# Performance work log

Hardware: AMD Instinct MI355X
Metric: run time of the kernel (lower is better)

Reference implementation:

```python
import itertools
import jax, jax.numpy as jnp
import numpy as np

B, N, ETA, K, Z, HID, NATOM, NBOND = 128, 40, 64, 32, 32, 256, 24, 5
A = B * N
E = B * (N * (N - 1) // 2)
TAU = 1.0  # gumbel_softmax_temperature default


def _bn(x, g, b, eps=1e-5):
    # BatchNorm1d in training mode: batch statistics, biased variance
    m = jnp.mean(x, axis=0)
    v = jnp.var(x, axis=0)
    return (x - m) * jax.lax.rsqrt(v + eps) * g + b


def _prelu(x, a):
    return jnp.where(x >= 0, x, a * x)


def _mlp(x, w1, b1, g, be, a, w2, b2):
    # Linear -> BatchNorm1d -> PReLU -> Linear
    return _prelu(_bn(x @ w1 + b1, g, be), a) @ w2 + b2


def setup_inputs() -> dict:
    key = jax.random.key(0)
    ks = jax.random.split(key, 16)
    # static all-pairs edge index per graph, offset per graph (mirrors decode_z)
    pairs = np.array(list(itertools.combinations(range(N), 2)), dtype=np.int64)  # [P,2]
    offs = (np.arange(B, dtype=np.int64) * N)[:, None, None]
    edge_index = jnp.asarray((pairs[None] + offs).reshape(-1, 2))  # [E,2]
    node_graph_idx = jnp.asarray(np.repeat(np.arange(B, dtype=np.int64), N))  # [A]

    def w(k, shape, fan_in):
        return jax.random.normal(k, shape, jnp.float32) / np.sqrt(fan_in).astype(np.float32)

    return {
        "eta": jax.random.normal(ks[0], (B, ETA), jnp.float32),
        "gumbel_u": jax.random.uniform(ks[1], (A, K), jnp.float32, 1e-6, 1.0 - 1e-6),
        "noise_z": jax.random.normal(ks[2], (A, Z), jnp.float32),
        "edge_index": edge_index,
        "node_graph_idx": node_graph_idx,
        # cluster_mlp
        "cw1": w(ks[3], (ETA, HID), ETA), "cb1": jnp.zeros(HID), "cg": jnp.ones(HID), "cbe": jnp.zeros(HID), "ca": jnp.float32(0.25),
        "cw2": w(ks[4], (HID, K), HID), "cb2": jnp.zeros(K),
        # mixture params (torch: randn means, zero log-sigmas)
        "cm": jax.random.normal(ks[5], (K, Z), jnp.float32), "cls": jnp.zeros((K, Z), jnp.float32),
        # atom_classifier
        "aw1": w(ks[6], (Z, HID), Z), "ab1": jnp.zeros(HID), "ag": jnp.ones(HID), "abe": jnp.zeros(HID), "aa": jnp.float32(0.25),
        "aw2": w(ks[7], (HID, NATOM), HID), "ab2": jnp.zeros(NATOM),
        # bond bilinear tensor [d, a, b]
        "bm": jax.random.normal(ks[8], (Z, Z, Z), jnp.float32) / np.sqrt(Z).astype(np.float32),
        # bond_type_mlp
        "bw1": w(ks[9], (Z, HID), Z), "bb1": jnp.zeros(HID), "bg": jnp.ones(HID), "bbe": jnp.zeros(HID), "ba": jnp.float32(0.25),
        "bw2": w(ks[10], (HID, NBOND), HID), "bb2": jnp.zeros(NBOND),
    }


def reference(eta, gumbel_u, noise_z, edge_index, node_graph_idx,
              cw1, cb1, cg, cbe, ca, cw2, cb2, cm, cls,
              aw1, ab1, ag, abe, aa, aw2, ab2,
              bm, bw1, bb1, bg, bbe, ba, bw2, bb2):
    # decode_eta: pi = softmax(cluster_mlp(eta)); log_pi = log(pi)
    log_pi = jax.nn.log_softmax(_mlp(eta, cw1, cb1, cg, cbe, ca, cw2, cb2), axis=1)
    # repeat_interleave(log_pi, num_atoms) -> per-atom logits
    logits = log_pi[node_graph_idx]  # [A, K]
    # gumbel_softmax hard=True (straight-through)
    g = -jnp.log(-jnp.log(gumbel_u))
    y_soft = jax.nn.softmax((logits + g) / TAU, axis=1)
    y_hard = jax.nn.one_hot(jnp.argmax(y_soft, axis=1), K, dtype=y_soft.dtype)
    c = y_hard - jax.lax.stop_gradient(y_soft) + y_soft  # [A, K]
    # select cluster mean / log-sigma, reparameterize
    mu = c @ cm                 # [A, Z]
    log_sigma = c @ cls         # [A, Z]
    z = noise_z * jnp.exp(jnp.clip(log_sigma, -20.0, 30.0)) + mu
    # decode_z
    atom_types = _mlp(z, aw1, ab1, ag, abe, aa, aw2, ab2)  # [A, NATOM]
    Wm = 0.5 * (bm + jnp.swapaxes(bm, 1, 2))  # symmetrize over (a, b)
    zi = z[edge_index[:, 0]]  # [E, Z]
    zj = z[edge_index[:, 1]]  # [E, Z]
    t = jnp.einsum('ea,dab->edb', zi, Wm)       # [E, Z, Z]
    edge_feat = jnp.einsum('edb,eb->ed', t, zj)  # z_i^T W_d z_j, [E, Z]
    edge_types = jax.nn.softmax(_mlp(edge_feat, bw1, bb1, bg, bbe, ba, bw2, bb2), axis=1)  # [E, NBOND]
    return atom_types, edge_types
```

## Files before the change

kernel.cpp:

```cpp
#include <hip/hip_runtime.h>
#include <math.h>

#define BG    128
#define NN    40
#define AK    32
#define ZD    32
#define HIDN  256
#define ETAD  64
#define NATOM 24
#define NBOND 5
#define NA    (BG*NN)
#define EPG   (NN*(NN-1)/2)
#define NE    (BG*EPG)

typedef __attribute__((ext_vector_type(8))) short bf16x8;
typedef __attribute__((ext_vector_type(4))) float f32x4;

__device__ __forceinline__ unsigned short f2bf(float f) {
    union { float f; unsigned int u; } x; x.f = f;
    unsigned int r = x.u + 0x7fffu + ((x.u >> 16) & 1u);
    return (unsigned short)(r >> 16);
}
__device__ __forceinline__ unsigned int pk2bf(float lo, float hi) {
    return (unsigned int)f2bf(lo) | ((unsigned int)f2bf(hi) << 16);
}

__global__ __launch_bounds__(256) void k_pre(const float* __restrict__ bm,
                                             const float* __restrict__ bw1,
                                             const float* __restrict__ aw1,
                                             const float* __restrict__ aw2,
                                             const float* __restrict__ eta,
                                             const float* __restrict__ cw1,
                                             const float* __restrict__ cb1,
                                             unsigned short* __restrict__ wmpk,
                                             unsigned short* __restrict__ bpack,
                                             unsigned short* __restrict__ apk1,
                                             unsigned short* __restrict__ apk2,
                                             float* __restrict__ h1,
                                             float* __restrict__ cpart,
                                             float* __restrict__ zacc) {
    int b = blockIdx.x, t = threadIdx.x;
    if (b < 128) {
        int idx = b*256 + t;
        int d = idx >> 10;
        int Bt = (idx >> 9) & 1, ln = (idx >> 3) & 63, j = idx & 7;
        int al = Bt*16 + (ln & 15);
        int be = (ln >> 4)*8 + j;
        float v = 0.5f * (bm[d*1024 + al*32 + be] + bm[d*1024 + be*32 + al]);
        wmpk[idx] = f2bf(v);
    } else if (b < 160) {
        int idx = (b - 128)*256 + t;
        int ct = idx >> 9, rem = idx & 511;
        int lane = rem >> 3, j = rem & 7;
        bpack[idx] = f2bf(bw1[((lane >> 4)*8 + j)*HIDN + ct*16 + (lane & 15)]);
    } else if (b < 192) {
        int idx = (b - 160)*256 + t;
        int ct = idx >> 9, rem = idx & 511;
        int lane = rem >> 3, j = rem & 7;
        apk1[idx] = f2bf(aw1[((lane >> 4)*8 + j)*HIDN + ct*16 + (lane & 15)]);
    } else if (b < 224) {
        int idx = (b - 192)*256 + t;
        int f = idx >> 9, rem = idx & 511;
        int lane = rem >> 3, j = rem & 7;
        int kc = f >> 1, ot = f & 1;
        int col = ot*16 + (lane & 15);
        int k = kc*32 + (lane >> 4)*8 + j;
        apk2[idx] = (col < NATOM) ? f2bf(aw2[k*NATOM + col]) : 0;
    } else if (b < 232) {
        __shared__ float es[16*ETAD];
        int b2 = b - 224;
        int r0 = b2*16;
        for (int i = t; i < 16*ETAD; i += 256) es[i] = eta[r0*ETAD + i];
        __syncthreads();
        int c = t;
        float bias = cb1[c], s = 0.f, ss = 0.f;
        for (int r = 0; r < 16; ++r) {
            float acc = bias;
#pragma unroll
            for (int a = 0; a < ETAD; ++a) acc += es[r*ETAD + a] * cw1[a*HIDN + c];
            h1[(r0 + r)*HIDN + c] = acc;
            s += acc; ss += acc*acc;
        }
        cpart[b2*512 + c] = s;
        cpart[b2*512 + 256 + c] = ss;
    } else {
        for (int i = t; i < 2112; i += 256) zacc[i] = 0.f;
    }
}

__global__ __launch_bounds__(256) void k_class_z(const float* __restrict__ h1,
                                                 const float* __restrict__ cpart,
                                                 const float* __restrict__ cg,
                                                 const float* __restrict__ cbe,
                                                 const float* __restrict__ ca,
                                                 const float* __restrict__ cw2,
                                                 const float* __restrict__ cb2,
                                                 const float* __restrict__ gum,
                                                 const float* __restrict__ noise,
                                                 const float* __restrict__ cm,
                                                 const float* __restrict__ cls,
                                                 float* __restrict__ z,
                                                 float* __restrict__ mom_z) {
    __shared__ float p[HIDN];
    __shared__ float vp2[256];
    __shared__ float oo[AK];
    __shared__ float lp[AK];
    __shared__ float zl[NN*36];
    int g = blockIdx.x, t = threadIdx.x;
    float aP = ca[0];
    {
        float s = 0.f, ss = 0.f;
#pragma unroll
        for (int b = 0; b < 8; ++b) { s += cpart[b*512 + t]; ss += cpart[b*512 + 256 + t]; }
        float m = s * (1.0f/(float)BG);
        float v = ss * (1.0f/(float)BG) - m*m;
        float x = h1[g*HIDN + t];
        float xn = (x - m) * (1.0f/sqrtf(v + 1e-5f)) * cg[t] + cbe[t];
        p[t] = xn >= 0.f ? xn : aP*xn;
    }
    __syncthreads();
    {
        int k = t & 31, part = t >> 5;
        float acc = 0.f;
        const float* pc = &p[part*32];
        const float* wc = &cw2[(part*32)*AK + k];
#pragma unroll
        for (int c = 0; c < 32; ++c) acc += pc[c] * wc[c*AK];
        vp2[t] = acc;
    }
    __syncthreads();
    if (t < AK) {
        float acc = cb2[t];
#pragma unroll
        for (int q = 0; q < 8; ++q) acc += vp2[q*32 + t];
        oo[t] = acc;
    }
    __syncthreads();
    if (t < AK) {
        float m = -INFINITY;
#pragma unroll
        for (int k = 0; k < AK; ++k) m = fmaxf(m, oo[k]);
        float S = 0.f;
#pragma unroll
        for (int k = 0; k < AK; ++k) S += expf(oo[k] - m);
        lp[t] = oo[t] - m - logf(S);
    }
    __syncthreads();
    int lane = t & 31;
#pragma unroll
    for (int nb = 0; nb < 5; ++nb) {
        int node = nb*8 + (t >> 5);
        int n = g*NN + node;
        float u = gum[(size_t)n*AK + lane];
        float x = lp[lane] - logf(-logf(u));
        float m = x;
#pragma unroll
        for (int s = 1; s < 32; s <<= 1) m = fmaxf(m, __shfl_xor(m, s, 32));
        float e = expf(x - m);
        float S = e;
#pragma unroll
        for (int s = 1; s < 32; s <<= 1) S += __shfl_xor(S, s, 32);
        unsigned long long bal = __ballot(x == m);
        unsigned grp = (unsigned)(bal >> (t & 32));
        int am = __ffs(grp) - 1;
        float best = 1.0f / S;
        float cam = (1.0f - best) + best;
        float ls = cam * cls[am*ZD + lane];
        ls = fminf(fmaxf(ls, -20.0f), 30.0f);
        float zv = noise[(size_t)n*ZD + lane]*expf(ls) + cam*cm[am*ZD + lane];
        z[(size_t)n*ZD + lane] = zv;
        zl[node*36 + lane] = zv;
    }
    __syncthreads();
    {
        int a = t >> 3, b4 = (t & 7) << 2;
        float ax = 0.f, ay = 0.f, az = 0.f, aw = 0.f;
        float mx = 0.f, my = 0.f, mz = 0.f, mw = 0.f;
        for (int r = 0; r < NN; ++r) {
            float  va = zl[r*36 + a];
            float4 vb = *(const float4*)&zl[r*36 + b4];
            ax += va*vb.x; ay += va*vb.y; az += va*vb.z; aw += va*vb.w;
            mx += vb.x;    my += vb.y;    mz += vb.z;    mw += vb.w;
        }
        atomicAdd(&mom_z[a*ZD + b4 + 0], ax);
        atomicAdd(&mom_z[a*ZD + b4 + 1], ay);
        atomicAdd(&mom_z[a*ZD + b4 + 2], az);
        atomicAdd(&mom_z[a*ZD + b4 + 3], aw);
        if (a == 0) {
            atomicAdd(&mom_z[ZD*ZD + b4 + 0], mx);
            atomicAdd(&mom_z[ZD*ZD + b4 + 1], my);
            atomicAdd(&mom_z[ZD*ZD + b4 + 2], mz);
            atomicAdd(&mom_z[ZD*ZD + b4 + 3], mw);
        }
    }
}

__global__ __launch_bounds__(256) void k_edge_feat(const float* __restrict__ z,
                                                   const unsigned short* __restrict__ wmpk,
                                                   float* __restrict__ ef) {
    __shared__ unsigned short zfrag[3*512];
    __shared__ unsigned short Tf[4][3*512];
    __shared__ float efl[EPG*9];
    int t = threadIdx.x;
    int g = blockIdx.x >> 2, dg = blockIdx.x & 3;

    if (t < 192) {
        int I = t >> 6, ln = t & 63;
        int row = I*16 + (ln & 15), c0 = (ln >> 4)*8;
        unsigned int pk[4] = {0u, 0u, 0u, 0u};
        if (row < NN) {
            const float* zp = &z[((size_t)g*NN + row)*ZD + c0];
            float4 v0 = *(const float4*)zp;
            float4 v1 = *(const float4*)(zp + 4);
            pk[0] = pk2bf(v0.x, v0.y); pk[1] = pk2bf(v0.z, v0.w);
            pk[2] = pk2bf(v1.x, v1.y); pk[3] = pk2bf(v1.z, v1.w);
        }
        *(uint4*)&zfrag[(I*64 + ln)*8] = make_uint4(pk[0], pk[1], pk[2], pk[3]);
    }
    __syncthreads();

    int w = t >> 6, lane = t & 63;
    int l15 = lane & 15, gq = lane >> 4;
    f32x4 zero4 = {0.f, 0.f, 0.f, 0.f};

    bf16x8 zf[3];
#pragma unroll
    for (int I = 0; I < 3; ++I) zf[I] = *(const bf16x8*)&zfrag[I*512 + lane*8];

    for (int dk = 0; dk < 2; ++dk) {
        int dd = w*2 + dk;
        int d  = dg*8 + dd;
        bf16x8 wA[2];
        wA[0] = *(const bf16x8*)&wmpk[(d*2 + 0)*512 + lane*8];
        wA[1] = *(const bf16x8*)&wmpk[(d*2 + 1)*512 + lane*8];

        unsigned short* tw = &Tf[w][0];
        int gqp_lo = (gq >> 1);
        int jo     = (gq & 1)*4;
#pragma unroll
        for (int Bt = 0; Bt < 2; ++Bt) {
#pragma unroll
            for (int I = 0; I < 3; ++I) {
                f32x4 c = __builtin_amdgcn_mfma_f32_16x16x32_bf16(wA[Bt], zf[I], zero4, 0, 0, 0);
                int gqp = Bt*2 + gqp_lo;
                int pos = I*512 + gqp*128 + l15*8 + jo;
                unsigned int d0 = pk2bf(c[0], c[1]);
                unsigned int d1 = pk2bf(c[2], c[3]);
                *(uint2*)&tw[pos] = make_uint2(d0, d1);
            }
        }
        __syncthreads();

        bf16x8 tf[3];
#pragma unroll
        for (int J = 0; J < 3; ++J) tf[J] = *(const bf16x8*)&Tf[w][J*512 + lane*8];

#pragma unroll
        for (int I = 0; I < 3; ++I) {
#pragma unroll
            for (int J = I; J < 3; ++J) {
                f32x4 gacc = __builtin_amdgcn_mfma_f32_16x16x32_bf16(zf[I], tf[J], zero4, 0, 0, 0);
                int j = J*16 + l15;
                if (j < NN) {
#pragma unroll
                    for (int r = 0; r < 4; ++r) {
                        int i = I*16 + 4*gq + r;
                        if (i < j) {
                            int e = i*(79 - i)/2 + (j - i - 1);
                            efl[e*9 + dd] = gacc[r];
                        }
                    }
                }
            }
        }
        __syncthreads();
    }

    size_t gE = (size_t)g * EPG;
    for (int idx = t; idx < EPG*8; idx += 256) {
        int e = idx >> 3, dd = idx & 7;
        ef[(gE + e)*ZD + dg*8 + dd] = efl[e*9 + dd];
    }
}

#define MOMB 192
__global__ __launch_bounds__(256) void k_moment(const float* __restrict__ src,
                                                float* __restrict__ mom, int nchunks) {
    __shared__ float sm[ZD*ZD + ZD];
    int t = threadIdx.x;
    for (int i = t; i < ZD*ZD + ZD; i += 256) sm[i] = 0.f;
    __syncthreads();
    int lane = t & 63, wv = t >> 6;
    int l15 = lane & 15, g4 = lane >> 4;
    int wgid = blockIdx.x * 4 + wv;
    const int nw = MOMB * 4;
    f32x4 aII = {0,0,0,0}, aIJ = {0,0,0,0}, aJI = {0,0,0,0}, aJJ = {0,0,0,0};
    float mI = 0.f, mJ = 0.f;
    for (int ch = wgid; ch < nchunks; ch += nw) {
        const float* p = src + ((size_t)ch*32 + g4*8)*ZD + l15;
        float vI[8], vJ[8];
#pragma unroll
        for (int j = 0; j < 8; ++j) { vI[j] = p[j*ZD]; vJ[j] = p[j*ZD + 16]; }
        bf16x8 fI, fJ;
#pragma unroll
        for (int j = 0; j < 8; ++j) {
            fI[j] = (short)f2bf(vI[j]); fJ[j] = (short)f2bf(vJ[j]);
            mI += vI[j]; mJ += vJ[j];
        }
        aII = __builtin_amdgcn_mfma_f32_16x16x32_bf16(fI, fI, aII, 0, 0, 0);
        aIJ = __builtin_amdgcn_mfma_f32_16x16x32_bf16(fI, fJ, aIJ, 0, 0, 0);
        aJI = __builtin_amdgcn_mfma_f32_16x16x32_bf16(fJ, fI, aJI, 0, 0, 0);
        aJJ = __builtin_amdgcn_mfma_f32_16x16x32_bf16(fJ, fJ, aJJ, 0, 0, 0);
    }
#pragma unroll
    for (int r = 0; r < 4; ++r) {
        int row = g4*4 + r;
        atomicAdd(&sm[row*ZD + l15],             aII[r]);
        atomicAdd(&sm[row*ZD + 16 + l15],        aIJ[r]);
        atomicAdd(&sm[(16 + row)*ZD + l15],      aJI[r]);
        atomicAdd(&sm[(16 + row)*ZD + 16 + l15], aJJ[r]);
    }
    atomicAdd(&sm[ZD*ZD + l15], mI);
    atomicAdd(&sm[ZD*ZD + 16 + l15], mJ);
    __syncthreads();
    for (int i = t; i < ZD*ZD + ZD; i += 256) atomicAdd(&mom[i], sm[i]);
}

__global__ __launch_bounds__(256) void k_prep2(const float* __restrict__ mom_z,
                                               const float* __restrict__ mom_ef,
                                               const float* __restrict__ aw1,
                                               const float* __restrict__ ab1,
                                               const float* __restrict__ ag,
                                               const float* __restrict__ abe,
                                               const float* __restrict__ bw1,
                                               const float* __restrict__ bb1,
                                               const float* __restrict__ bg,
                                               const float* __restrict__ bbe,
                                               float* __restrict__ ascale,
                                               float* __restrict__ ashift,
                                               float* __restrict__ bscale,
                                               float* __restrict__ bshift) {
    bool bond = blockIdx.x >= 8;
    const float* mom = bond ? mom_ef : mom_z;
    const float* w1  = bond ? bw1 : aw1;
    const float* b1  = bond ? bb1 : ab1;
    const float* g   = bond ? bg  : ag;
    const float* be  = bond ? bbe : abe;
    float inv_n      = bond ? (1.0f/(float)NE) : (1.0f/(float)NA);
    float* scale     = bond ? bscale : ascale;
    float* shift     = bond ? bshift : ashift;

    __shared__ float mean[ZD];
    __shared__ float cov[ZD*ZD];
    __shared__ float vp[256], mp[256];
    int t = threadIdx.x;
    if (t < ZD) mean[t] = mom[ZD*ZD + t] * inv_n;
    __syncthreads();
    for (int pp = t; pp < ZD*ZD; pp += 256) {
        int a = pp >> 5, b = pp & 31;
        cov[pp] = mom[pp] * inv_n - mean[a]*mean[b];
    }
    __syncthreads();
    int c = (blockIdx.x & 7) * 32 + (t & 31);
    int part = t >> 5;
    float wr[ZD];
#pragma unroll
    for (int b = 0; b < ZD; ++b) wr[b] = w1[b*HIDN + c];
    float var = 0.f, mh = 0.f;
#pragma unroll
    for (int q = 0; q < 4; ++q) {
        int a = part*4 + q;
        float tmp = 0.f;
#pragma unroll
        for (int b = 0; b < ZD; ++b) tmp += cov[a*ZD + b] * wr[b];
        var += tmp * wr[a];
        mh  += mean[a] * wr[a];
    }
    vp[t] = var; mp[t] = mh;
    __syncthreads();
    if (t < 32) {
        float v = 0.f, m = 0.f;
#pragma unroll
        for (int q = 0; q < 8; ++q) { v += vp[q*32 + t]; m += mp[q*32 + t]; }
        m += b1[c];
        float rs = rsqrtf(fmaxf(v, 0.f) + 1e-5f) * g[c];
        scale[c] = rs;
        shift[c] = be[c] - m * rs;
    }
}

#define PSH 264
#define ATOMB (NA/64)
#define BROWS4 128
__global__ __launch_bounds__(256) void k_out(const float* __restrict__ z,
                                             const unsigned short* __restrict__ apk1,
                                             const unsigned short* __restrict__ apk2,
                                             const float* __restrict__ ab1,
                                             const float* __restrict__ ascale,
                                             const float* __restrict__ ashift,
                                             const float* __restrict__ aa,
                                             const float* __restrict__ ab2,
                                             const float* __restrict__ ef,
                                             const unsigned short* __restrict__ bpack,
                                             const float* __restrict__ bb1,
                                             const float* __restrict__ bscale,
                                             const float* __restrict__ bshift,
                                             const float* __restrict__ ba,
                                             const float* __restrict__ bw2,
                                             const float* __restrict__ bb2,
                                             float* __restrict__ out_atom,
                                             float* __restrict__ out_bond) {
    __shared__ unsigned short smu[4*16*PSH];
    int t = threadIdx.x;
    int w = t >> 6, lane = t & 63;
    int l15 = lane & 15, gq = lane >> 4;
    f32x4 zero4 = {0.f, 0.f, 0.f, 0.f};

    if (blockIdx.x < ATOMB) {
        size_t r0 = (size_t)blockIdx.x * 64 + (size_t)w * 16;
        float aP = aa[0];
        unsigned short* ptw = &smu[w*16*PSH];

        const float* zp = &z[(r0 + l15)*ZD + gq*8];
        float4 z0 = *(const float4*)zp;
        float4 z1 = *(const float4*)(zp + 4);
        bf16x8 af;
        af[0] = (short)f2bf(z0.x); af[1] = (short)f2bf(z0.y);
        af[2] = (short)f2bf(z0.z); af[3] = (short)f2bf(z0.w);
        af[4] = (short)f2bf(z1.x); af[5] = (short)f2bf(z1.y);
        af[6] = (short)f2bf(z1.z); af[7] = (short)f2bf(z1.w);

#pragma unroll
        for (int ct = 0; ct < 16; ++ct) {
            bf16x8 bf = *(const bf16x8*)&apk1[ct*512 + lane*8];
            f32x4 c = __builtin_amdgcn_mfma_f32_16x16x32_bf16(af, bf, zero4, 0, 0, 0);
            int ch = ct*16 + l15;
            float sc = ascale[ch];
            float sh = ashift[ch] + ab1[ch]*sc;
#pragma unroll
            for (int r = 0; r < 4; ++r) {
                float xn = c[r]*sc + sh;
                float pv = xn >= 0.f ? xn : aP*xn;
                ptw[(4*gq + r)*PSH + ch] = f2bf(pv);
            }
        }

        f32x4 o0 = zero4, o1 = zero4;
#pragma unroll
        for (int kc = 0; kc < 8; ++kc) {
            bf16x8 af2 = *(const bf16x8*)&ptw[l15*PSH + kc*32 + gq*8];
            bf16x8 b0 = *(const bf16x8*)&apk2[(kc*2 + 0)*512 + lane*8];
            bf16x8 b1 = *(const bf16x8*)&apk2[(kc*2 + 1)*512 + lane*8];
            o0 = __builtin_amdgcn_mfma_f32_16x16x32_bf16(af2, b0, o0, 0, 0, 0);
            o1 = __builtin_amdgcn_mfma_f32_16x16x32_bf16(af2, b1, o1, 0, 0, 0);
        }
#pragma unroll
        for (int r = 0; r < 4; ++r) {
            size_t row = r0 + 4*gq + r;
            out_atom[row*NATOM + l15] = o0[r] + ab2[l15];
            if (l15 < 8) out_atom[row*NATOM + 16 + l15] = o1[r] + ab2[16 + l15];
        }
        return;
    }

    float* w2s = (float*)smu;
    float* scs = w2s + HIDN*NBOND;
    float* shs = scs + HIDN;
    size_t r0 = (size_t)(blockIdx.x - ATOMB) * BROWS4;

    for (int i = t; i < HIDN*NBOND; i += 256) w2s[i] = bw2[i];
    { float sc = bscale[t]; scs[t] = sc; shs[t] = bshift[t] + bb1[t]*sc; }
    __syncthreads();

    float aP = ba[0];
    float b2r[NBOND];
#pragma unroll
    for (int k = 0; k < NBOND; ++k) b2r[k] = bb2[k];

#pragma unroll
    for (int rt = 0; rt < 2; ++rt) {
        size_t rowt = r0 + (size_t)(w*2 + rt)*16;
        const float* ar = &ef[(rowt + l15)*ZD + gq*8];
        float4 a0 = *(const float4*)ar;
        float4 a1 = *(const float4*)(ar + 4);
        bf16x8 af;
        af[0] = (short)f2bf(a0.x); af[1] = (short)f2bf(a0.y);
        af[2] = (short)f2bf(a0.z); af[3] = (short)f2bf(a0.w);
        af[4] = (short)f2bf(a1.x); af[5] = (short)f2bf(a1.y);
        af[6] = (short)f2bf(a1.z); af[7] = (short)f2bf(a1.w);

        float part[4][NBOND];
#pragma unroll
        for (int r = 0; r < 4; ++r)
#pragma unroll
            for (int k = 0; k < NBOND; ++k) part[r][k] = 0.f;

#pragma unroll
        for (int h = 0; h < 2; ++h) {
            bf16x8 bfr[8];
#pragma unroll
            for (int q = 0; q < 8; ++q)
                bfr[q] = *(const bf16x8*)&bpack[(h*8 + q)*512 + lane*8];
            f32x4 acc[8];
#pragma unroll
            for (int q = 0; q < 8; ++q)
                acc[q] = __builtin_amdgcn_mfma_f32_16x16x32_bf16(af, bfr[q], zero4, 0, 0, 0);
#pragma unroll
            for (int q = 0; q < 8; ++q) {
                int c = (h*8 + q)*16 + l15;
                float sc = scs[c], sh = shs[c];
                float w0 = w2s[c*NBOND+0], w1v = w2s[c*NBOND+1], w2v = w2s[c*NBOND+2];
                float w3 = w2s[c*NBOND+3], w4 = w2s[c*NBOND+4];
#pragma unroll
                for (int r = 0; r < 4; ++r) {
                    float xn = acc[q][r]*sc + sh;
                    float pv = xn >= 0.f ? xn : aP*xn;
                    part[r][0] += pv*w0; part[r][1] += pv*w1v; part[r][2] += pv*w2v;
                    part[r][3] += pv*w3; part[r][4] += pv*w4;
                }
            }
        }

#pragma unroll
        for (int s = 1; s < 16; s <<= 1) {
#pragma unroll
            for (int r = 0; r < 4; ++r)
#pragma unroll
                for (int k = 0; k < NBOND; ++k)
                    part[r][k] += __shfl_xor(part[r][k], s, 64);
        }

        if (l15 == 0) {
#pragma unroll
            for (int r = 0; r < 4; ++r) {
                size_t row = rowt + gq*4 + r;
                float lg[NBOND];
                float m = -INFINITY;
#pragma unroll
                for (int k = 0; k < NBOND; ++k) { lg[k] = part[r][k] + b2r[k]; m = fmaxf(m, lg[k]); }
                float S = 0.f;
#pragma unroll
                for (int k = 0; k < NBOND; ++k) { lg[k] = expf(lg[k] - m); S += lg[k]; }
                float invS = 1.f / S;
#pragma unroll
                for (int k = 0; k < NBOND; ++k) out_bond[row*NBOND + k] = lg[k] * invS;
            }
        }
    }
}

extern "C" void kernel_launch(void* const* d_in, const int* in_sizes, int n_in,
                              void* d_out, int out_size, void* d_ws, size_t ws_size,
                              hipStream_t stream) {
    (void)in_sizes; (void)n_in; (void)out_size; (void)ws_size;
    const float* eta  = (const float*)d_in[0];
    const float* gum  = (const float*)d_in[1];
    const float* noi  = (const float*)d_in[2];
    const float* cw1  = (const float*)d_in[5];
    const float* cb1  = (const float*)d_in[6];
    const float* cg   = (const float*)d_in[7];
    const float* cbe  = (const float*)d_in[8];
    const float* ca   = (const float*)d_in[9];
    const float* cw2  = (const float*)d_in[10];
    const float* cb2  = (const float*)d_in[11];
    const float* cm   = (const float*)d_in[12];
    const float* cls  = (const float*)d_in[13];
    const float* aw1  = (const float*)d_in[14];
    const float* ab1  = (const float*)d_in[15];
    const float* ag   = (const float*)d_in[16];
    const float* abe  = (const float*)d_in[17];
    const float* aa   = (const float*)d_in[18];
    const float* aw2  = (const float*)d_in[19];
    const float* ab2  = (const float*)d_in[20];
    const float* bm   = (const float*)d_in[21];
    const float* bw1  = (const float*)d_in[22];
    const float* bb1  = (const float*)d_in[23];
    const float* bg   = (const float*)d_in[24];
    const float* bbe  = (const float*)d_in[25];
    const float* ba   = (const float*)d_in[26];
    const float* bw2  = (const float*)d_in[27];
    const float* bb2  = (const float*)d_in[28];
    float* out = (float*)d_out;
    float* ws  = (float*)d_ws;

    float*          mom_z  = ws;
    float*          mom_ef = ws + 1056;
    float*          ascale = ws + 2112;
    float*          ashift = ws + 2368;
    float*          bscale = ws + 2624;
    float*          bshift = ws + 2880;
    float*          cpart  = ws + 3136;
    unsigned short* bpack  = (unsigned short*)(ws + 7232);
    unsigned short* apk1   = (unsigned short*)(ws + 11328);
    unsigned short* apk2   = (unsigned short*)(ws + 15424);
    unsigned short* wmpk   = (unsigned short*)(ws + 19520);
    float*          h1     = ws + 35904;
    float*          zbuf   = ws + 68672;
    float*          efb    = ws + 232512;

    k_pre      <<<dim3(233),      dim3(256), 0, stream>>>(bm, bw1, aw1, aw2, eta, cw1, cb1,
                                                          wmpk, bpack, apk1, apk2, h1, cpart, ws);
    k_class_z  <<<dim3(BG),       dim3(256), 0, stream>>>(h1, cpart, cg, cbe, ca, cw2, cb2,
                                                          gum, noi, cm, cls, zbuf, mom_z);
    k_edge_feat<<<dim3(4*BG),     dim3(256), 0, stream>>>(zbuf, wmpk, efb);
    k_moment   <<<dim3(MOMB),     dim3(256), 0, stream>>>(efb, mom_ef, NE/32);
    k_prep2    <<<dim3(16),       dim3(256), 0, stream>>>(mom_z, mom_ef, aw1, ab1, ag, abe,
                                                          bw1, bb1, bg, bbe,
                                                          ascale, ashift, bscale, bshift);
    k_out      <<<dim3(ATOMB + NE/BROWS4), dim3(256), 0, stream>>>(
                                                          zbuf, apk1, apk2, ab1, ascale, ashift,
                                                          aa, ab2,
                                                          efb, bpack, bb1, bscale, bshift,
                                                          ba, bw2, bb2,
                                                          out, out + NA*NATOM);
}
```

Before: 84.12 us.

## Spread class_z over more blocks, move z moments into moment kernel, shrink edge tiles

k_class_z now runs five blocks per graph, each handling eight nodes. The block-level z moment accumulation and its atomics are removed from it; those moments are instead computed by extra blocks appended to k_moment, which reuse the MFMA moment path over zbuf. In k_edge_feat, the per-iteration barriers inside the d loop are replaced by a single barrier after the loop. k_out's bond tiles are halved so each wave handles one 16-row tile and the grid doubles. The intent is more parallelism and less serial work per block, at the cost of recomputing the cluster MLP head five times per graph. Dropping the inner barriers is a possible race risk, since the Tf write/read sequence is per-wave and the loop may overwrite Tf on its next iteration.

```diff
diff --git a/kernel.cpp b/kernel.cpp
--- a/kernel.cpp
+++ b/kernel.cpp
@@ -99,19 +99,19 @@
                                                  const float* __restrict__ noise,
                                                  const float* __restrict__ cm,
                                                  const float* __restrict__ cls,
-                                                 float* __restrict__ z,
-                                                 float* __restrict__ mom_z) {
+                                                 float* __restrict__ z) {
     __shared__ float p[HIDN];
     __shared__ float vp2[256];
     __shared__ float oo[AK];
     __shared__ float lp[AK];
-    __shared__ float zl[NN*36];
-    int g = blockIdx.x, t = threadIdx.x;
+    int t = threadIdx.x;
+    int g = blockIdx.x / 5, q = blockIdx.x % 5;
     float aP = ca[0];
+
     {
         float s = 0.f, ss = 0.f;
 #pragma unroll
-        for (int b = 0; b < 8; ++b) { s += cpart[b*512 + t]; ss += cpart[b*512 + 256 + t]; }
+        for (int qq = 0; qq < 8; ++qq) { s += cpart[qq*512 + t]; ss += cpart[qq*512 + 256 + t]; }
         float m = s * (1.0f/(float)BG);
         float v = ss * (1.0f/(float)BG) - m*m;
         float x = h1[g*HIDN + t];
@@ -132,7 +132,7 @@
     if (t < AK) {
         float acc = cb2[t];
 #pragma unroll
-        for (int q = 0; q < 8; ++q) acc += vp2[q*32 + t];
+        for (int qq = 0; qq < 8; ++qq) acc += vp2[qq*32 + t];
         oo[t] = acc;
     }
     __syncthreads();
@@ -146,10 +146,9 @@
         lp[t] = oo[t] - m - logf(S);
     }
     __syncthreads();
-    int lane = t & 31;
-#pragma unroll
-    for (int nb = 0; nb < 5; ++nb) {
-        int node = nb*8 + (t >> 5);
+    {
+        int lane = t & 31;
+        int node = q*8 + (t >> 5);
         int n = g*NN + node;
         float u = gum[(size_t)n*AK + lane];
         float x = lp[lane] - logf(-logf(u));
@@ -167,31 +166,7 @@
         float cam = (1.0f - best) + best;
         float ls = cam * cls[am*ZD + lane];
         ls = fminf(fmaxf(ls, -20.0f), 30.0f);
-        float zv = noise[(size_t)n*ZD + lane]*expf(ls) + cam*cm[am*ZD + lane];
-        z[(size_t)n*ZD + lane] = zv;
-        zl[node*36 + lane] = zv;
-    }
-    __syncthreads();
-    {
-        int a = t >> 3, b4 = (t & 7) << 2;
-        float ax = 0.f, ay = 0.f, az = 0.f, aw = 0.f;
-        float mx = 0.f, my = 0.f, mz = 0.f, mw = 0.f;
-        for (int r = 0; r < NN; ++r) {
-            float  va = zl[r*36 + a];
-            float4 vb = *(const float4*)&zl[r*36 + b4];
-            ax += va*vb.x; ay += va*vb.y; az += va*vb.z; aw += va*vb.w;
-            mx += vb.x;    my += vb.y;    mz += vb.z;    mw += vb.w;
-        }
-        atomicAdd(&mom_z[a*ZD + b4 + 0], ax);
-        atomicAdd(&mom_z[a*ZD + b4 + 1], ay);
-        atomicAdd(&mom_z[a*ZD + b4 + 2], az);
-        atomicAdd(&mom_z[a*ZD + b4 + 3], aw);
-        if (a == 0) {
-            atomicAdd(&mom_z[ZD*ZD + b4 + 0], mx);
-            atomicAdd(&mom_z[ZD*ZD + b4 + 1], my);
-            atomicAdd(&mom_z[ZD*ZD + b4 + 2], mz);
-            atomicAdd(&mom_z[ZD*ZD + b4 + 3], mw);
-        }
+        z[(size_t)n*ZD + lane] = noise[(size_t)n*ZD + lane]*expf(ls) + cam*cm[am*ZD + lane];
     }
 }
 
@@ -249,7 +224,6 @@
                 *(uint2*)&tw[pos] = make_uint2(d0, d1);
             }
         }
-        __syncthreads();
 
         bf16x8 tf[3];
 #pragma unroll
@@ -273,8 +247,8 @@
                 }
             }
         }
-        __syncthreads();
-    }
+    }
+    __syncthreads();
 
     size_t gE = (size_t)g * EPG;
     for (int idx = t; idx < EPG*8; idx += 256) {
@@ -284,16 +258,25 @@
 }
 
 #define MOMB 192
-__global__ __launch_bounds__(256) void k_moment(const float* __restrict__ src,
-                                                float* __restrict__ mom, int nchunks) {
+#define ZMB  40
+__global__ __launch_bounds__(256) void k_moment(const float* __restrict__ efsrc,
+                                                const float* __restrict__ zsrc,
+                                                float* __restrict__ mom_ef,
+                                                float* __restrict__ mom_z) {
     __shared__ float sm[ZD*ZD + ZD];
     int t = threadIdx.x;
+    bool isz = blockIdx.x >= MOMB;
+    const float* src = isz ? zsrc : efsrc;
+    float* mom = isz ? mom_z : mom_ef;
+    int nchunks = isz ? (NA/32) : (NE/32);
+    int bid = isz ? (blockIdx.x - MOMB) : blockIdx.x;
+    int nw = (isz ? ZMB : MOMB) * 4;
+
     for (int i = t; i < ZD*ZD + ZD; i += 256) sm[i] = 0.f;
     __syncthreads();
     int lane = t & 63, wv = t >> 6;
     int l15 = lane & 15, g4 = lane >> 4;
-    int wgid = blockIdx.x * 4 + wv;
-    const int nw = MOMB * 4;
+    int wgid = bid * 4 + wv;
     f32x4 aII = {0,0,0,0}, aIJ = {0,0,0,0}, aJI = {0,0,0,0}, aJJ = {0,0,0,0};
     float mI = 0.f, mJ = 0.f;
     for (int ch = wgid; ch < nchunks; ch += nw) {
@@ -391,7 +374,7 @@
 
 #define PSH 264
 #define ATOMB (NA/64)
-#define BROWS4 128
+#define BROWS4 64
 __global__ __launch_bounds__(256) void k_out(const float* __restrict__ z,
                                              const unsigned short* __restrict__ apk1,
                                              const unsigned short* __restrict__ apk2,
@@ -477,74 +460,71 @@
 #pragma unroll
     for (int k = 0; k < NBOND; ++k) b2r[k] = bb2[k];
 
-#pragma unroll
-    for (int rt = 0; rt < 2; ++rt) {
-        size_t rowt = r0 + (size_t)(w*2 + rt)*16;
-        const float* ar = &ef[(rowt + l15)*ZD + gq*8];
-        float4 a0 = *(const float4*)ar;
-        float4 a1 = *(const float4*)(ar + 4);
-        bf16x8 af;
-        af[0] = (short)f2bf(a0.x); af[1] = (short)f2bf(a0.y);
-        af[2] = (short)f2bf(a0.z); af[3] = (short)f2bf(a0.w);
-        af[4] = (short)f2bf(a1.x); af[5] = (short)f2bf(a1.y);
-        af[6] = (short)f2bf(a1.z); af[7] = (short)f2bf(a1.w);
-
-        float part[4][NBOND];
+    size_t rowt = r0 + (size_t)w*16;
+    const float* ar = &ef[(rowt + l15)*ZD + gq*8];
+    float4 a0 = *(const float4*)ar;
+    float4 a1 = *(const float4*)(ar + 4);
+    bf16x8 af;
+    af[0] = (short)f2bf(a0.x); af[1] = (short)f2bf(a0.y);
+    af[2] = (short)f2bf(a0.z); af[3] = (short)f2bf(a0.w);
+    af[4] = (short)f2bf(a1.x); af[5] = (short)f2bf(a1.y);
+    af[6] = (short)f2bf(a1.z); af[7] = (short)f2bf(a1.w);
+
+    float part[4][NBOND];
+#pragma unroll
+    for (int r = 0; r < 4; ++r)
+#pragma unroll
+        for (int k = 0; k < NBOND; ++k) part[r][k] = 0.f;
+
+#pragma unroll
+    for (int h = 0; h < 2; ++h) {
+        bf16x8 bfr[8];
+#pragma unroll
+        for (int q = 0; q < 8; ++q)
+            bfr[q] = *(const bf16x8*)&bpack[(h*8 + q)*512 + lane*8];
+        f32x4 acc[8];
+#pragma unroll
+        for (int q = 0; q < 8; ++q)
+            acc[q] = __builtin_amdgcn_mfma_f32_16x16x32_bf16(af, bfr[q], zero4, 0, 0, 0);
+#pragma unroll
+        for (int q = 0; q < 8; ++q) {
+            int c = (h*8 + q)*16 + l15;
+            float sc = scs[c], sh = shs[c];
+            float w0 = w2s[c*NBOND+0], w1v = w2s[c*NBOND+1], w2v = w2s[c*NBOND+2];
+            float w3 = w2s[c*NBOND+3], w4 = w2s[c*NBOND+4];
+#pragma unroll
+            for (int r = 0; r < 4; ++r) {
+                float xn = acc[q][r]*sc + sh;
+                float pv = xn >= 0.f ? xn : aP*xn;
+                part[r][0] += pv*w0; part[r][1] += pv*w1v; part[r][2] += pv*w2v;
+                part[r][3] += pv*w3; part[r][4] += pv*w4;
+            }
+        }
+    }
+
+#pragma unroll
+    for (int s = 1; s < 16; s <<= 1) {
 #pragma unroll
         for (int r = 0; r < 4; ++r)
 #pragma unroll
-            for (int k = 0; k < NBOND; ++k) part[r][k] = 0.f;
-
-#pragma unroll
-        for (int h = 0; h < 2; ++h) {
-            bf16x8 bfr[8];
-#pragma unroll
-            for (int q = 0; q < 8; ++q)
-                bfr[q] = *(const bf16x8*)&bpack[(h*8 + q)*512 + lane*8];
-            f32x4 acc[8];
-#pragma unroll
-            for (int q = 0; q < 8; ++q)
-                acc[q] = __builtin_amdgcn_mfma_f32_16x16x32_bf16(af, bfr[q], zero4, 0, 0, 0);
-#pragma unroll
-            for (int q = 0; q < 8; ++q) {
-                int c = (h*8 + q)*16 + l15;
-                float sc = scs[c], sh = shs[c];
-                float w0 = w2s[c*NBOND+0], w1v = w2s[c*NBOND+1], w2v = w2s[c*NBOND+2];
-                float w3 = w2s[c*NBOND+3], w4 = w2s[c*NBOND+4];
-#pragma unroll
-                for (int r = 0; r < 4; ++r) {
-                    float xn = acc[q][r]*sc + sh;
-                    float pv = xn >= 0.f ? xn : aP*xn;
-                    part[r][0] += pv*w0; part[r][1] += pv*w1v; part[r][2] += pv*w2v;
-                    part[r][3] += pv*w3; part[r][4] += pv*w4;
-                }
-            }
-        }
-
-#pragma unroll
-        for (int s = 1; s < 16; s <<= 1) {
-#pragma unroll
-            for (int r = 0; r < 4; ++r)
-#pragma unroll
-                for (int k = 0; k < NBOND; ++k)
-                    part[r][k] += __shfl_xor(part[r][k], s, 64);
-        }
-
-        if (l15 == 0) {
-#pragma unroll
-            for (int r = 0; r < 4; ++r) {
-                size_t row = rowt + gq*4 + r;
-                float lg[NBOND];
-                float m = -INFINITY;
-#pragma unroll
-                for (int k = 0; k < NBOND; ++k) { lg[k] = part[r][k] + b2r[k]; m = fmaxf(m, lg[k]); }
-                float S = 0.f;
-#pragma unroll
-                for (int k = 0; k < NBOND; ++k) { lg[k] = expf(lg[k] - m); S += lg[k]; }
-                float invS = 1.f / S;
-#pragma unroll
-                for (int k = 0; k < NBOND; ++k) out_bond[row*NBOND + k] = lg[k] * invS;
-            }
+            for (int k = 0; k < NBOND; ++k)
+                part[r][k] += __shfl_xor(part[r][k], s, 64);
+    }
+
+    if (l15 == 0) {
+#pragma unroll
+        for (int r = 0; r < 4; ++r) {
+            size_t row = rowt + gq*4 + r;
+            float lg[NBOND];
+            float m = -INFINITY;
+#pragma unroll
+            for (int k = 0; k < NBOND; ++k) { lg[k] = part[r][k] + b2r[k]; m = fmaxf(m, lg[k]); }
+            float S = 0.f;
+#pragma unroll
+            for (int k = 0; k < NBOND; ++k) { lg[k] = expf(lg[k] - m); S += lg[k]; }
+            float invS = 1.f / S;
+#pragma unroll
+            for (int k = 0; k < NBOND; ++k) out_bond[row*NBOND + k] = lg[k] * invS;
         }
     }
 }
@@ -558,7 +538,7 @@
     const float* noi  = (const float*)d_in[2];
     const float* cw1  = (const float*)d_in[5];
     const float* cb1  = (const float*)d_in[6];
-    const float* cg   = (const float*)d_in[7];
+    const float* cgp  = (const float*)d_in[7];
     const float* cbe  = (const float*)d_in[8];
     const float* ca   = (const float*)d_in[9];
     const float* cw2  = (const float*)d_in[10];
@@ -598,19 +578,19 @@
     float*          zbuf   = ws + 68672;
     float*          efb    = ws + 232512;
 
-    k_pre      <<<dim3(233),      dim3(256), 0, stream>>>(bm, bw1, aw1, aw2, eta, cw1, cb1,
-                                                          wmpk, bpack, apk1, apk2, h1, cpart, ws);
-    k_class_z  <<<dim3(BG),       dim3(256), 0, stream>>>(h1, cpart, cg, cbe, ca, cw2, cb2,
-                                                          gum, noi, cm, cls, zbuf, mom_z);
-    k_edge_feat<<<dim3(4*BG),     dim3(256), 0, stream>>>(zbuf, wmpk, efb);
-    k_moment   <<<dim3(MOMB),     dim3(256), 0, stream>>>(efb, mom_ef, NE/32);
-    k_prep2    <<<dim3(16),       dim3(256), 0, stream>>>(mom_z, mom_ef, aw1, ab1, ag, abe,
-                                                          bw1, bb1, bg, bbe,
-                                                          ascale, ashift, bscale, bshift);
+    k_pre      <<<dim3(233),       dim3(256), 0, stream>>>(bm, bw1, aw1, aw2, eta, cw1, cb1,
+                                                           wmpk, bpack, apk1, apk2, h1, cpart, ws);
+    k_class_z  <<<dim3(5*BG),      dim3(256), 0, stream>>>(h1, cpart, cgp, cbe, ca, cw2, cb2,
+                                                           gum, noi, cm, cls, zbuf);
+    k_edge_feat<<<dim3(4*BG),      dim3(256), 0, stream>>>(zbuf, wmpk, efb);
+    k_moment   <<<dim3(MOMB+ZMB),  dim3(256), 0, stream>>>(efb, zbuf, mom_ef, mom_z);
+    k_prep2    <<<dim3(16),        dim3(256), 0, stream>>>(mom_z, mom_ef, aw1, ab1, ag, abe,
+                                                           bw1, bb1, bg, bbe,
+                                                           ascale, ashift, bscale, bshift);
     k_out      <<<dim3(ATOMB + NE/BROWS4), dim3(256), 0, stream>>>(
-                                                          zbuf, apk1, apk2, ab1, ascale, ashift,
-                                                          aa, ab2,
-                                                          efb, bpack, bb1, bscale, bshift,
-                                                          ba, bw2, bb2,
-                                                          out, out + NA*NATOM);
-}
+                                                           zbuf, apk1, apk2, ab1, ascale, ashift,
+                                                           aa, ab2,
+                                                           efb, bpack, bb1, bscale, bshift,
+                                                           ba, bw2, bb2,
+                                                           out, out + NA*NATOM);
+}
```

New measurement: 71.81 us (median of 2 runs). 14.6% less time.
